# Performance work log

Measured on AMD Instinct MI355X. Metric: run time of the kernel, lower is better.

## Reference

```python
import jax, jax.numpy as jnp
import numpy as np

B, S, F, H, O = 1024, 512, 18, 64, 15
BN_EPS = 1e-5


def setup_inputs() -> dict:
    key = jax.random.key(0)
    ks = jax.random.split(key, 12)
    bound = 1.0 / np.sqrt(H)  # torch LSTM/Linear init range

    def u(k, shape):
        return jax.random.uniform(k, shape, jnp.float32, -bound, bound)

    return {
        "X": jax.random.normal(ks[0], (B, S, F), jnp.float32),
        # torch nn.LSTM gate layout: [i, f, g, o] stacked along dim 0 -> [4H, in]
        "W_ih0": u(ks[1], (4 * H, F)),
        "W_hh0": u(ks[2], (4 * H, H)),
        "b_ih0": u(ks[3], (4 * H,)),
        "b_hh0": u(ks[4], (4 * H,)),
        "W_ih1": u(ks[5], (4 * H, H)),
        "W_hh1": u(ks[6], (4 * H, H)),
        "b_ih1": u(ks[7], (4 * H,)),
        "b_hh1": u(ks[8], (4 * H,)),
        "bn_gamma": jnp.ones((H,), jnp.float32),
        "bn_beta": jnp.zeros((H,), jnp.float32),
        "cls_W": u(ks[9], (O, H)),
        "cls_b": u(ks[10], (O,)),
    }


def _lstm_layer(x, W_ih, W_hh, b_ih, b_hh):
    """Single LSTM layer, batch_first input x: [B, S, in] -> [B, S, H]."""
    Hh = W_hh.shape[1]
    # Precompute input-to-gate projections for the whole sequence: [S, B, 4H]
    xg = jnp.einsum('bsf,gf->sbg', x, W_ih) + b_ih + b_hh

    def step(carry, gx):
        h, c = carry
        g = gx + h @ W_hh.T  # [B, 4H]
        i, f, gg, o = jnp.split(g, 4, axis=-1)
        i = jax.nn.sigmoid(i)
        f = jax.nn.sigmoid(f)
        gg = jnp.tanh(gg)
        o = jax.nn.sigmoid(o)
        c = f * c + i * gg
        h = o * jnp.tanh(c)
        return (h, c), h

    h0 = jnp.zeros((x.shape[0], Hh), x.dtype)
    _, hs = jax.lax.scan(step, (h0, h0), xg)
    return jnp.transpose(hs, (1, 0, 2))  # [B, S, H]


def reference(X, W_ih0, W_hh0, b_ih0, b_hh0, W_ih1, W_hh1, b_ih1, b_hh1,
              bn_gamma, bn_beta, cls_W, cls_b):
    h1 = _lstm_layer(X, W_ih0, W_hh0, b_ih0, b_hh0)
    # inter-layer dropout is identity in eval / deterministic reference
    h2 = _lstm_layer(h1, W_ih1, W_hh1, b_ih1, b_hh1)
    last = h2[:, -1, :]  # [B, H]
    # BatchNorm1d in training mode: batch statistics over the batch dim
    mean = jnp.mean(last, axis=0)
    var = jnp.var(last, axis=0)
    normalized = (last - mean) * jax.lax.rsqrt(var + BN_EPS) * bn_gamma + bn_beta
    # final dropout = identity (deterministic)
    return normalized @ cls_W.T + cls_b  # [B, O]
```

## Files before the change

kernel.cpp:

```cpp
#include <hip/hip_runtime.h>
#include <cstdint>
#include <cstddef>

#define B_SZ  1024
#define S_LEN 512
#define NH    64

typedef float f32x2 __attribute__((ext_vector_type(2)));
typedef float f32x4 __attribute__((ext_vector_type(4)));

__device__ __forceinline__ float sigmoid_f(float x) {
    return __fdividef(1.0f, 1.0f + __expf(-x));
}
__device__ __forceinline__ float tanh_f(float x) {
    return 1.0f - __fdividef(2.0f, __expf(2.0f * x) + 1.0f);
}
__device__ __forceinline__ void pk_fma(f32x2& acc, f32x2 a, f32x2 b) {
    asm("v_pk_fma_f32 %0, %1, %2, %0" : "+v"(acc) : "v"(a), "v"(b));
}
template<int CTRL>
__device__ __forceinline__ float dpp_add(float x) {
    int s = __builtin_amdgcn_update_dpp(0, __float_as_int(x), CTRL, 0xF, 0xF, true);
    return x + __int_as_float(s);
}

template<int KIN>
__global__ __launch_bounds__(256, 2) void lstm_scan(
    const float* __restrict__ xin,
    const float* __restrict__ W_ih,
    const float* __restrict__ W_hh,
    const float* __restrict__ b_ih,
    const float* __restrict__ b_hh,
    float* __restrict__ h_all,
    float* __restrict__ h_last)
{
    constexpr int K     = KIN + NH;
    constexpr int KP    = (K + 31) & ~31;
    constexpr int CH    = KP / 8;
    constexpr int STAG  = (CH % 8 == 0) ? 4 : 0;
    constexpr int CROW  = CH + STAG;
    constexpr int NB128 = CH / 4;

    __shared__ __align__(16) float in_lds[8 * CROW];
    __shared__ float g_part[520];

    const int t  = threadIdx.x;
    const int kc = t & 7;
    const int gg = t >> 3;
    const int b  = blockIdx.x;

    auto WPOS = [](int f) { return (f / CH) * CROW + (f % CH); };

    f32x2 w2[8][CH / 2];
    #pragma unroll
    for (int j = 0; j < 8; ++j) {
        const int g = 8 * gg + j;
        #pragma unroll
        for (int i = 0; i < CH; ++i) {
            const int k = kc * CH + i;
            float wv;
            if (k < KIN)    wv = W_ih[g * KIN + k];
            else if (k < K) wv = W_hh[g * NH + (k - KIN)];
            else            wv = 0.0f;
            w2[j][i >> 1][i & 1] = wv;
        }
    }

    float bias_i = 0, bias_f = 0, bias_g = 0, bias_o = 0, cst = 0.0f;
    if (t < NH) {
        bias_i = b_ih[0 * NH + t] + b_hh[0 * NH + t];
        bias_f = b_ih[1 * NH + t] + b_hh[1 * NH + t];
        bias_g = b_ih[2 * NH + t] + b_hh[2 * NH + t];
        bias_o = b_ih[3 * NH + t] + b_hh[3 * NH + t];
    }

    if (t < 8 * CROW) in_lds[t] = 0.0f;
    __syncthreads();
    if (t >= 64 && t < 64 + KIN)
        in_lds[WPOS(t - 64)] = xin[(size_t)b * S_LEN * KIN + (t - 64)];
    __syncthreads();

    const int ib = kc * CROW;

    for (int s = 0; s < S_LEN; ++s) {
        float xreg = 0.0f;
        if (t >= 64 && t < 64 + KIN && s + 1 < S_LEN)
            xreg = xin[(size_t)b * S_LEN * KIN + (size_t)(s + 1) * KIN + (t - 64)];

        f32x2 acc2[8] = {};
        #pragma unroll
        for (int ii = 0; ii < NB128; ++ii) {
            const f32x4 v = *reinterpret_cast<const f32x4*>(&in_lds[ib + 4 * ii]);
            const f32x2 vlo = {v.x, v.y};
            const f32x2 vhi = {v.z, v.w};
            #pragma unroll
            for (int j = 0; j < 8; ++j) {
                pk_fma(acc2[j], w2[j][2 * ii],     vlo);
                pk_fma(acc2[j], w2[j][2 * ii + 1], vhi);
            }
        }
        float a[8];
        #pragma unroll
        for (int j = 0; j < 8; ++j) a[j] = acc2[j].x + acc2[j].y;
        #pragma unroll
        for (int j = 0; j < 8; ++j) a[j] = dpp_add<0xB1>(a[j]);
        #pragma unroll
        for (int j = 0; j < 8; ++j) a[j] = dpp_add<0x4E>(a[j]);
        {
            const int sel = kc & 3;
            const float q01 = (sel & 1) ? a[1] : a[0];
            const float q23 = (sel & 1) ? a[3] : a[2];
            const float lo  = (sel & 2) ? q23 : q01;
            const float q45 = (sel & 1) ? a[5] : a[4];
            const float q67 = (sel & 1) ? a[7] : a[6];
            const float hi  = (sel & 2) ? q67 : q45;
            g_part[t]       = lo;
            g_part[t + 260] = hi;
        }
        __syncthreads();

        if (t < NH) {
            const int jj = t;
            const int wb = 8 * (jj >> 3) + (jj & 3) + ((jj & 4) ? 260 : 0);
            const float pi = g_part[0 * 64 + wb] + g_part[0 * 64 + wb + 4] + bias_i;
            const float pf = g_part[1 * 64 + wb] + g_part[1 * 64 + wb + 4] + bias_f;
            const float pg = g_part[2 * 64 + wb] + g_part[2 * 64 + wb + 4] + bias_g;
            const float po = g_part[3 * 64 + wb] + g_part[3 * 64 + wb + 4] + bias_o;
            const float iv = sigmoid_f(pi);
            const float fv = sigmoid_f(pf);
            const float gv = tanh_f(pg);
            const float ov = sigmoid_f(po);
            cst = fmaf(fv, cst, iv * gv);
            const float hv = ov * tanh_f(cst);
            in_lds[WPOS(KIN + jj)] = hv;
            if (h_all)
                h_all[((size_t)b * S_LEN + s) * NH + jj] = hv;
            if (h_last && s == S_LEN - 1)
                h_last[(size_t)b * NH + jj] = hv;
        } else if (t < 64 + KIN) {
            if (s + 1 < S_LEN) in_lds[WPOS(t - 64)] = xreg;
        }
        __syncthreads();
    }
}

__global__ void bn_stats_kernel(const float* __restrict__ last,
                                const float* __restrict__ gamma,
                                const float* __restrict__ beta,
                                float* __restrict__ scale,
                                float* __restrict__ shift)
{
    const int jf = blockIdx.x;
    const int t  = threadIdx.x;
    float s1 = 0.0f, s2 = 0.0f;
    for (int b = t; b < B_SZ; b += 256) {
        const float v = last[b * NH + jf];
        s1 += v; s2 += v * v;
    }
    #pragma unroll
    for (int off = 32; off > 0; off >>= 1) {
        s1 += __shfl_down(s1, off, 64);
        s2 += __shfl_down(s2, off, 64);
    }
    __shared__ float ls1[4], ls2[4];
    if ((t & 63) == 0) { ls1[t >> 6] = s1; ls2[t >> 6] = s2; }
    __syncthreads();
    if (t == 0) {
        const float S1 = ls1[0] + ls1[1] + ls1[2] + ls1[3];
        const float S2 = ls2[0] + ls2[1] + ls2[2] + ls2[3];
        const float mean = S1 * (1.0f / B_SZ);
        const float var  = S2 * (1.0f / B_SZ) - mean * mean;
        const float sc   = gamma[jf] * rsqrtf(var + 1e-5f);
        scale[jf] = sc;
        shift[jf] = beta[jf] - mean * sc;
    }
}

__global__ void cls_kernel(const float* __restrict__ last,
                           const float* __restrict__ scale,
                           const float* __restrict__ shift,
                           const float* __restrict__ W,
                           const float* __restrict__ bias,
                           float* __restrict__ out)
{
    const int t  = threadIdx.x;
    const int o  = t & 15;
    const int ry = t >> 4;
    const int b  = blockIdx.x * 16 + ry;
    if (o >= 15) return;
    float acc = bias[o];
    #pragma unroll
    for (int jf = 0; jf < NH; ++jf) {
        const float nv = fmaf(last[b * NH + jf], scale[jf], shift[jf]);
        acc = fmaf(nv, W[o * NH + jf], acc);
    }
    out[b * 15 + o] = acc;
}

extern "C" void kernel_launch(void* const* d_in, const int* in_sizes, int n_in,
                              void* d_out, int out_size, void* d_ws, size_t ws_size,
                              hipStream_t stream) {
    const float* X      = (const float*)d_in[0];
    const float* W_ih0  = (const float*)d_in[1];
    const float* W_hh0  = (const float*)d_in[2];
    const float* b_ih0  = (const float*)d_in[3];
    const float* b_hh0  = (const float*)d_in[4];
    const float* W_ih1  = (const float*)d_in[5];
    const float* W_hh1  = (const float*)d_in[6];
    const float* b_ih1  = (const float*)d_in[7];
    const float* b_hh1  = (const float*)d_in[8];
    const float* gamma  = (const float*)d_in[9];
    const float* beta   = (const float*)d_in[10];
    const float* cls_W  = (const float*)d_in[11];
    const float* cls_b  = (const float*)d_in[12];
    float* out = (float*)d_out;

    float* h1    = (float*)d_ws;
    float* last  = h1 + (size_t)B_SZ * S_LEN * NH;
    float* scale = last + (size_t)B_SZ * NH;
    float* shift = scale + NH;

    lstm_scan<18><<<B_SZ, 256, 0, stream>>>(
        X, W_ih0, W_hh0, b_ih0, b_hh0, h1, nullptr);
    lstm_scan<64><<<B_SZ, 256, 0, stream>>>(
        h1, W_ih1, W_hh1, b_ih1, b_hh1, nullptr, last);
    bn_stats_kernel<<<NH, 256, 0, stream>>>(last, gamma, beta, scale, shift);
    cls_kernel<<<B_SZ / 16, 256, 0, stream>>>(last, scale, shift, cls_W, cls_b, out);
}
```

Baseline: 1.690 ms.

## Process two batch rows per block with 512 threads and halved per-thread weights

Each block now handles two batch sequences with 512 threads. Each thread holds weights for 4 gate rows instead of 8 and reuses them across both sequences. This cuts per-thread register pressure, raises the launch-bounds occupancy target, and halves the grid while keeping the total thread count. The trade-off is that barriers now span 512 threads, and an empty asm keeps the weights pinned in registers.

```diff
diff --git a/kernel.cpp b/kernel.cpp
--- a/kernel.cpp
+++ b/kernel.cpp
@@ -25,7 +25,7 @@
 }
 
 template<int KIN>
-__global__ __launch_bounds__(256, 2) void lstm_scan(
+__global__ __launch_bounds__(512, 4) void lstm_scan(
     const float* __restrict__ xin,
     const float* __restrict__ W_ih,
     const float* __restrict__ W_hh,
@@ -34,27 +34,29 @@
     float* __restrict__ h_all,
     float* __restrict__ h_last)
 {
+    constexpr int R     = 2;
     constexpr int K     = KIN + NH;
     constexpr int KP    = (K + 31) & ~31;
     constexpr int CH    = KP / 8;
     constexpr int STAG  = (CH % 8 == 0) ? 4 : 0;
     constexpr int CROW  = CH + STAG;
-    constexpr int NB128 = CH / 4;
-
-    __shared__ __align__(16) float in_lds[8 * CROW];
-    __shared__ float g_part[520];
+    constexpr int NB    = CH / 4;
+    constexpr int ROWW  = 8 * CROW;
+
+    __shared__ __align__(16) float in_lds[R][ROWW];
+    __shared__ float g_part[R][512];
 
     const int t  = threadIdx.x;
     const int kc = t & 7;
     const int gg = t >> 3;
-    const int b  = blockIdx.x;
+    const int b0 = blockIdx.x * R;
 
     auto WPOS = [](int f) { return (f / CH) * CROW + (f % CH); };
 
-    f32x2 w2[8][CH / 2];
+    f32x2 w2[4][CH / 2];
     #pragma unroll
-    for (int j = 0; j < 8; ++j) {
-        const int g = 8 * gg + j;
+    for (int j = 0; j < 4; ++j) {
+        const int g = 4 * gg + j;
         #pragma unroll
         for (int i = 0; i < CH; ++i) {
             const int k = kc * CH + i;
@@ -67,78 +69,97 @@
     }
 
     float bias_i = 0, bias_f = 0, bias_g = 0, bias_o = 0, cst = 0.0f;
-    if (t < NH) {
-        bias_i = b_ih[0 * NH + t] + b_hh[0 * NH + t];
-        bias_f = b_ih[1 * NH + t] + b_hh[1 * NH + t];
-        bias_g = b_ih[2 * NH + t] + b_hh[2 * NH + t];
-        bias_o = b_ih[3 * NH + t] + b_hh[3 * NH + t];
-    }
-
-    if (t < 8 * CROW) in_lds[t] = 0.0f;
+    if (t < R * NH) {
+        const int jj = t & 63;
+        bias_i = b_ih[0 * NH + jj] + b_hh[0 * NH + jj];
+        bias_f = b_ih[1 * NH + jj] + b_hh[1 * NH + jj];
+        bias_g = b_ih[2 * NH + jj] + b_hh[2 * NH + jj];
+        bias_o = b_ih[3 * NH + jj] + b_hh[3 * NH + jj];
+    }
+
+    for (int i = t; i < R * ROWW; i += 512) ((float*)in_lds)[i] = 0.0f;
     __syncthreads();
-    if (t >= 64 && t < 64 + KIN)
-        in_lds[WPOS(t - 64)] = xin[(size_t)b * S_LEN * KIN + (t - 64)];
+    if (t >= 128 && t < 128 + R * KIN) {
+        const int xt = t - 128, r = xt / KIN, f = xt - (xt / KIN) * KIN;
+        in_lds[r][WPOS(f)] = xin[(size_t)(b0 + r) * S_LEN * KIN + f];
+    }
     __syncthreads();
 
     const int ib = kc * CROW;
 
     for (int s = 0; s < S_LEN; ++s) {
+        #pragma unroll
+        for (int j = 0; j < 4; ++j)
+            #pragma unroll
+            for (int i = 0; i < CH / 2; ++i)
+                asm volatile("" : "+v"(w2[j][i]));
+
         float xreg = 0.0f;
-        if (t >= 64 && t < 64 + KIN && s + 1 < S_LEN)
-            xreg = xin[(size_t)b * S_LEN * KIN + (size_t)(s + 1) * KIN + (t - 64)];
-
-        f32x2 acc2[8] = {};
-        #pragma unroll
-        for (int ii = 0; ii < NB128; ++ii) {
-            const f32x4 v = *reinterpret_cast<const f32x4*>(&in_lds[ib + 4 * ii]);
-            const f32x2 vlo = {v.x, v.y};
-            const f32x2 vhi = {v.z, v.w};
-            #pragma unroll
-            for (int j = 0; j < 8; ++j) {
-                pk_fma(acc2[j], w2[j][2 * ii],     vlo);
-                pk_fma(acc2[j], w2[j][2 * ii + 1], vhi);
+        if (t >= 128 && t < 128 + R * KIN && s + 1 < S_LEN) {
+            const int xt = t - 128, r = xt / KIN, f = xt - (xt / KIN) * KIN;
+            xreg = xin[(size_t)(b0 + r) * S_LEN * KIN + (size_t)(s + 1) * KIN + f];
+        }
+
+        float a[R][4];
+        #pragma unroll
+        for (int r = 0; r < R; ++r) {
+            f32x2 acc[4] = {};
+            #pragma unroll
+            for (int ii = 0; ii < NB; ++ii) {
+                const f32x4 v = *reinterpret_cast<const f32x4*>(&in_lds[r][ib + 4 * ii]);
+                const f32x2 vlo = {v.x, v.y};
+                const f32x2 vhi = {v.z, v.w};
+                #pragma unroll
+                for (int j = 0; j < 4; ++j) {
+                    pk_fma(acc[j], w2[j][2 * ii],     vlo);
+                    pk_fma(acc[j], w2[j][2 * ii + 1], vhi);
+                }
             }
-        }
-        float a[8];
-        #pragma unroll
-        for (int j = 0; j < 8; ++j) a[j] = acc2[j].x + acc2[j].y;
-        #pragma unroll
-        for (int j = 0; j < 8; ++j) a[j] = dpp_add<0xB1>(a[j]);
-        #pragma unroll
-        for (int j = 0; j < 8; ++j) a[j] = dpp_add<0x4E>(a[j]);
+            #pragma unroll
+            for (int j = 0; j < 4; ++j) a[r][j] = acc[j].x + acc[j].y;
+        }
+        #pragma unroll
+        for (int r = 0; r < R; ++r) {
+            #pragma unroll
+            for (int j = 0; j < 4; ++j) a[r][j] = dpp_add<0xB1>(a[r][j]);
+            #pragma unroll
+            for (int j = 0; j < 4; ++j) a[r][j] = dpp_add<0x4E>(a[r][j]);
+        }
         {
             const int sel = kc & 3;
-            const float q01 = (sel & 1) ? a[1] : a[0];
-            const float q23 = (sel & 1) ? a[3] : a[2];
-            const float lo  = (sel & 2) ? q23 : q01;
-            const float q45 = (sel & 1) ? a[5] : a[4];
-            const float q67 = (sel & 1) ? a[7] : a[6];
-            const float hi  = (sel & 2) ? q67 : q45;
-            g_part[t]       = lo;
-            g_part[t + 260] = hi;
+            #pragma unroll
+            for (int r = 0; r < R; ++r) {
+                const float v01 = (sel & 1) ? a[r][1] : a[r][0];
+                const float v23 = (sel & 1) ? a[r][3] : a[r][2];
+                g_part[r][t] = (sel & 2) ? v23 : v01;
+            }
         }
         __syncthreads();
 
-        if (t < NH) {
-            const int jj = t;
-            const int wb = 8 * (jj >> 3) + (jj & 3) + ((jj & 4) ? 260 : 0);
-            const float pi = g_part[0 * 64 + wb] + g_part[0 * 64 + wb + 4] + bias_i;
-            const float pf = g_part[1 * 64 + wb] + g_part[1 * 64 + wb + 4] + bias_f;
-            const float pg = g_part[2 * 64 + wb] + g_part[2 * 64 + wb + 4] + bias_g;
-            const float po = g_part[3 * 64 + wb] + g_part[3 * 64 + wb + 4] + bias_o;
+        if (t < R * NH) {
+            const int r  = t >> 6;
+            const int jj = t & 63;
+            const int w8 = 8 * (jj >> 2) + (jj & 3);
+            const float pi = g_part[r][0 * 128 + w8] + g_part[r][0 * 128 + w8 + 4] + bias_i;
+            const float pf = g_part[r][1 * 128 + w8] + g_part[r][1 * 128 + w8 + 4] + bias_f;
+            const float pg = g_part[r][2 * 128 + w8] + g_part[r][2 * 128 + w8 + 4] + bias_g;
+            const float po = g_part[r][3 * 128 + w8] + g_part[r][3 * 128 + w8 + 4] + bias_o;
             const float iv = sigmoid_f(pi);
             const float fv = sigmoid_f(pf);
             const float gv = tanh_f(pg);
             const float ov = sigmoid_f(po);
             cst = fmaf(fv, cst, iv * gv);
             const float hv = ov * tanh_f(cst);
-            in_lds[WPOS(KIN + jj)] = hv;
+            in_lds[r][WPOS(KIN + jj)] = hv;
             if (h_all)
-                h_all[((size_t)b * S_LEN + s) * NH + jj] = hv;
+                h_all[((size_t)(b0 + r) * S_LEN + s) * NH + jj] = hv;
             if (h_last && s == S_LEN - 1)
-                h_last[(size_t)b * NH + jj] = hv;
-        } else if (t < 64 + KIN) {
-            if (s + 1 < S_LEN) in_lds[WPOS(t - 64)] = xreg;
+                h_last[(size_t)(b0 + r) * NH + jj] = hv;
+        } else if (t < 128 + R * KIN) {
+            if (s + 1 < S_LEN) {
+                const int xt = t - 128, r = xt / KIN, f = xt - (xt / KIN) * KIN;
+                in_lds[r][WPOS(f)] = xreg;
+            }
         }
         __syncthreads();
     }
@@ -220,9 +241,9 @@
     float* scale = last + (size_t)B_SZ * NH;
     float* shift = scale + NH;
 
-    lstm_scan<18><<<B_SZ, 256, 0, stream>>>(
+    lstm_scan<18><<<B_SZ / 2, 512, 0, stream>>>(
         X, W_ih0, W_hh0, b_ih0, b_hh0, h1, nullptr);
-    lstm_scan<64><<<B_SZ, 256, 0, stream>>>(
+    lstm_scan<64><<<B_SZ / 2, 512, 0, stream>>>(
         h1, W_ih1, W_hh1, b_ih1, b_hh1, nullptr, last);
     bn_stats_kernel<<<NH, 256, 0, stream>>>(last, gamma, beta, scale, shift);
     cls_kernel<<<B_SZ / 16, 256, 0, stream>>>(last, scale, shift, cls_W, cls_b, out);
```

New measurement: 1.827 ms. +8.1%, slower.
